# Optimization experiments

Hardware: AMD Instinct MI355X
Metric: run time of the kernel (lower is better)

The kernel has to match this reference:

```python
import jax, jax.numpy as jnp
import numpy as np

NODE_DIM = 128
DEPTH = 4
N_NODES = 10000
N_EDGES = 320000


def setup_inputs() -> dict:
    key = jax.random.key(0)
    ks = jax.random.split(key, 12)
    s = 0.05
    D = NODE_DIM
    inp = {
        'h': jax.random.normal(ks[0], (N_NODES, D), jnp.float32),
        'x': jax.random.normal(ks[1], (N_NODES, 3), jnp.float32),
        'edges': jax.random.randint(ks[2], (2, N_EDGES), 0, N_NODES, jnp.int32),
        # edge_mlp: Linear(2D+1 -> D), SiLU, Linear(D -> D), SiLU  (per layer)
        'edge_w1': jax.random.normal(ks[3], (DEPTH, 2 * D + 1, D), jnp.float32) * s,
        'edge_b1': jnp.zeros((DEPTH, D), jnp.float32),
        'edge_w2': jax.random.normal(ks[4], (DEPTH, D, D), jnp.float32) * s,
        'edge_b2': jnp.zeros((DEPTH, D), jnp.float32),
        # node_mlp: Linear(2D -> D), SiLU, Linear(D -> D)  (per layer)
        'node_w1': jax.random.normal(ks[5], (DEPTH, 2 * D, D), jnp.float32) * s,
        'node_b1': jnp.zeros((DEPTH, D), jnp.float32),
        'node_w2': jax.random.normal(ks[6], (DEPTH, D, D), jnp.float32) * s,
        'node_b2': jnp.zeros((DEPTH, D), jnp.float32),
        # coord_mlp (only used by last layer, update_coords=True):
        # Linear(D -> D), SiLU, Linear(D -> 1, bias=False)
        'coord_w1': jax.random.normal(ks[7], (D, D), jnp.float32) * s,
        'coord_b1': jnp.zeros((D,), jnp.float32),
        'coord_w2': jax.random.normal(ks[8], (D, 1), jnp.float32) * s,
    }
    return inp


def reference(h, x, edges, edge_w1, edge_b1, edge_w2, edge_b2,
              node_w1, node_b1, node_w2, node_b2,
              coord_w1, coord_b1, coord_w2):
    silu = jax.nn.silu
    row, col = edges[0], edges[1]
    n = h.shape[0]
    for i in range(DEPTH):
        # coord2radial
        coord_diff = x[row] - x[col]                       # [E, 3]
        radial = jnp.sum(coord_diff * coord_diff, axis=-1, keepdims=True)  # [E, 1]
        # edge_model: m_ij = edge_mlp([h_i, h_j, radial])
        feat = jnp.concatenate([h[row], h[col], radial], axis=-1)  # [E, 2D+1]
        m = silu(feat @ edge_w1[i] + edge_b1[i])
        m = silu(m @ edge_w2[i] + edge_b2[i])              # [E, D]
        # coord_model (only last layer, coords_agg='mean')
        if i == DEPTH - 1:
            w = silu(m @ coord_w1 + coord_b1) @ coord_w2   # [E, 1]
            trans = coord_diff * w                          # [E, 3]
            agg = jax.ops.segment_sum(trans, row, num_segments=n)
            cnt = jax.ops.segment_sum(jnp.ones((row.shape[0], 1), trans.dtype),
                                      row, num_segments=n)
            x = x + agg / jnp.maximum(cnt, 1.0)
        # node_model: h = h + node_mlp([h, sum_j m_ij])  (residual=True)
        magg = jax.ops.segment_sum(m, row, num_segments=n)  # [N, D]
        hin = jnp.concatenate([h, magg], axis=-1)           # [N, 2D]
        out = silu(hin @ node_w1[i] + node_b1[i]) @ node_w2[i] + node_b2[i]
        h = h + out
    return h, x
```

## Files before the change

### kernel.cpp

```cpp
#include <hip/hip_runtime.h>

#define NND 10000
#define NE  320000
#define DD  128
#define NDEPTH 4
#define TE  64

typedef __attribute__((ext_vector_type(8))) short s8b;
typedef __attribute__((ext_vector_type(4))) float f4;
typedef unsigned short u16;
typedef unsigned int   u32;

__device__ __forceinline__ u16 f2b(float f) {
    u32 u = __builtin_bit_cast(u32, f);
    u32 r = (u + 0x7fffu + ((u >> 16) & 1u)) >> 16;
    return (u16)r;
}

__device__ __forceinline__ float b2f(u16 b) {
    u32 u = (u32)b << 16;
    return __builtin_bit_cast(float, u);
}

__device__ __forceinline__ u32 cvt_pk(float lo, float hi) {
    u32 r;
    asm("v_cvt_pk_bf16_f32 %0, %1, %2" : "=v"(r) : "v"(lo), "v"(hi));
    return r;
}

__device__ __forceinline__ float silu_f(float v) {
    return v / (1.0f + __expf(-v));
}

__device__ __forceinline__ s8b frag_a(const u16* rowp, int g) {
    union { s8b v; uint2 u2[2]; } r;
    r.u2[0] = *(const uint2*)(rowp + 4 * g);
    r.u2[1] = *(const uint2*)(rowp + 16 + 4 * g);
    return r.v;
}

__device__ __forceinline__ f4 mfma16(s8b a, s8b b, f4 c) {
    return __builtin_amdgcn_mfma_f32_16x16x32_bf16(a, b, c, 0, 0, 0);
}

__global__ __launch_bounds__(256) void egnn_pack(
    const float* __restrict__ ew1, const float* __restrict__ ew2,
    const float* __restrict__ nw1, const float* __restrict__ nw2,
    const float* __restrict__ cw1, u16* __restrict__ pw)
{
    int t = blockIdx.x * 256 + threadIdx.x;
    if (t >= 25 * 16384) return;
    int mat = t >> 14;
    int r   = t & 16383;
    int kt  = r >> 12;
    int nt  = (r >> 9) & 7;
    int lane= (r >> 3) & 63;
    int j   = r & 7;
    int g = lane >> 4, l15 = lane & 15;
    int k = kt * 32 + ((j < 4) ? (4 * g + j) : (16 + 4 * g + (j - 4)));
    int n = nt * 16 + l15;
    float v;
    if (mat < 24) {
        int layer = mat / 6, tp = mat % 6;
        switch (tp) {
            case 0: v = ew1[((size_t)layer * 257 + k) * DD + n]; break;
            case 1: v = ew1[((size_t)layer * 257 + 128 + k) * DD + n]; break;
            case 2: v = ew2[((size_t)layer * 128 + k) * DD + n]; break;
            case 3: v = nw1[((size_t)layer * 256 + k) * DD + n]; break;
            case 4: v = nw1[((size_t)layer * 256 + 128 + k) * DD + n]; break;
            default: v = nw2[((size_t)layer * 128 + k) * DD + n]; break;
        }
    } else {
        v = cw1[(size_t)k * DD + n];
    }
    pw[t] = f2b(v);
}

__global__ __launch_bounds__(256) void egnn_init(
    const float* __restrict__ h, u16* __restrict__ hb)
{
    int i = blockIdx.x * 256 + threadIdx.x;
    size_t base = (size_t)i * 4;
    if (base >= (size_t)NND * DD) return;
    float4 v = *(const float4*)(h + base);
    union { u16 s[4]; uint2 u; } t2;
    t2.s[0] = f2b(v.x); t2.s[1] = f2b(v.y); t2.s[2] = f2b(v.z); t2.s[3] = f2b(v.w);
    *(uint2*)(hb + base) = t2.u;
}

__global__ __launch_bounds__(256) void egnn_count(
    const int* __restrict__ edges, int* __restrict__ cnts)
{
    int e = blockIdx.x * 256 + threadIdx.x;
    if (e < NE) atomicAdd(&cnts[edges[e]], 1);
}

__global__ __launch_bounds__(1024) void egnn_scan(
    const int* __restrict__ cnts, int* __restrict__ off, int* __restrict__ cursor)
{
    __shared__ int part[1024];
    const int t = threadIdx.x;
    const int base = t * 10;
    int s = 0;
    #pragma unroll
    for (int j = 0; j < 10; ++j) {
        int i = base + j;
        s += (i < NND) ? cnts[i] : 0;
    }
    part[t] = s;
    __syncthreads();
    for (int d = 1; d < 1024; d <<= 1) {
        int v = (t >= d) ? part[t - d] : 0;
        __syncthreads();
        part[t] += v;
        __syncthreads();
    }
    int run = (t == 0) ? 0 : part[t - 1];
    #pragma unroll
    for (int j = 0; j < 10; ++j) {
        int i = base + j;
        if (i <= NND) { off[i] = run; cursor[i] = run; }
        if (i < NND) run += cnts[i];
    }
}

__global__ __launch_bounds__(256) void egnn_scatter(
    const int* __restrict__ edges, int* __restrict__ cursor,
    int* __restrict__ perm, int* __restrict__ rowsorted)
{
    int e = blockIdx.x * 256 + threadIdx.x;
    if (e >= NE) return;
    int r = edges[e];
    int p = atomicAdd(&cursor[r], 1);
    perm[p] = e;
    rowsorted[p] = r;
}

__global__ __launch_bounds__(256) void egnn_pre0(
    const u16* __restrict__ hb, const u16* __restrict__ pw,
    float* __restrict__ Pb, float* __restrict__ Qb)
{
    __shared__ __attribute__((aligned(16))) u16 tH[64][136];
    const int tid = threadIdx.x;
    const int n0  = blockIdx.x * 64;

    #pragma unroll
    for (int it = 0; it < 4; ++it) {
        int idx = tid + it * 256;
        int el = idx >> 4, part = idx & 15;
        int node = n0 + el;
        if (node < NND) {
            *(uint4*)&tH[el][part * 8] = *(const uint4*)(hb + (size_t)node * DD + part * 8);
        } else {
            uint4 z = {0u, 0u, 0u, 0u};
            *(uint4*)&tH[el][part * 8] = z;
        }
    }
    __syncthreads();

    const int wv = tid >> 6, lane = tid & 63;
    const int g = lane >> 4, l15 = lane & 15;
    const int wrow = wv * 16;

    f4 accP[8], accQ[8];
    #pragma unroll
    for (int nt = 0; nt < 8; ++nt) { accP[nt] = f4{0.f,0.f,0.f,0.f}; accQ[nt] = f4{0.f,0.f,0.f,0.f}; }
    const u16* pwa = pw;
    const u16* pwb = pw + 16384;
    #pragma unroll
    for (int kt = 0; kt < 4; ++kt) {
        s8b a = frag_a(&tH[wrow + l15][kt * 32], g);
        const u16* ba = pwa + (size_t)kt * 4096 + lane * 8;
        const u16* bb = pwb + (size_t)kt * 4096 + lane * 8;
        #pragma unroll
        for (int nt = 0; nt < 8; ++nt) {
            accP[nt] = mfma16(a, *(const s8b*)(ba + nt * 512), accP[nt]);
            accQ[nt] = mfma16(a, *(const s8b*)(bb + nt * 512), accQ[nt]);
        }
    }
    #pragma unroll
    for (int nt = 0; nt < 8; ++nt) {
        int n = nt * 16 + l15;
        #pragma unroll
        for (int r = 0; r < 4; ++r) {
            int node = n0 + wrow + g * 4 + r;
            if (node < NND) {
                Pb[(size_t)node * DD + n] = accP[nt][r];
                Qb[(size_t)node * DD + n] = accQ[nt][r];
            }
        }
    }
}

__global__ __launch_bounds__(256, 6) void egnn_edge(
    const float* __restrict__ Pb, const float* __restrict__ Qb,
    const float* __restrict__ xin,
    const int* __restrict__ edges,
    const int* __restrict__ perm, const int* __restrict__ rowsorted,
    const u16* __restrict__ pw,
    const float* __restrict__ ew1, const float* __restrict__ eb1,
    const float* __restrict__ eb2, const float* __restrict__ cb1,
    const float* __restrict__ cw2,
    float* __restrict__ magg, float* __restrict__ aggx,
    int layer, int last)
{
    __shared__ __attribute__((aligned(16))) u16 tA[TE][136];
    __shared__ float rad[TE];
    __shared__ float cdf[TE][3];
    __shared__ int   ridx[TE];
    __shared__ int   cidx[TE];
    __shared__ unsigned char segflag[TE + 1];

    const int tid = threadIdx.x;
    const int p0  = blockIdx.x * TE;

    if (tid < TE) {
        int p = p0 + tid;
        int e = perm[p];
        int r = rowsorted[p];
        int c = edges[NE + e];
        ridx[tid] = r; cidx[tid] = c;
        float d0 = xin[r * 3 + 0] - xin[c * 3 + 0];
        float d1 = xin[r * 3 + 1] - xin[c * 3 + 1];
        float d2 = xin[r * 3 + 2] - xin[c * 3 + 2];
        rad[tid] = d0 * d0 + d1 * d1 + d2 * d2;
        cdf[tid][0] = d0; cdf[tid][1] = d1; cdf[tid][2] = d2;
    }
    __syncthreads();

    if (tid < TE) {
        segflag[tid] = (tid == 0) || (ridx[tid] != ridx[tid - 1]);
        if (tid == 0) segflag[TE] = 1;
    }

    {
        const int cg = tid & 15;
        const int rg = tid >> 4;
        const float* b1p = eb1 + (size_t)layer * DD + cg * 8;
        const float* wrp = ew1 + ((size_t)layer * 257 + 256) * DD + cg * 8;
        float4 b0 = *(const float4*)(b1p);
        float4 b4 = *(const float4*)(b1p + 4);
        float4 w0 = *(const float4*)(wrp);
        float4 w4 = *(const float4*)(wrp + 4);
        #pragma unroll
        for (int k = 0; k < 4; ++k) {
            int row = rg + 16 * k;
            int rn = ridx[row], cn = cidx[row];
            float rd = rad[row];
            const float* pp = Pb + (size_t)rn * DD + cg * 8;
            const float* qq = Qb + (size_t)cn * DD + cg * 8;
            float4 pa = *(const float4*)(pp);
            float4 pc = *(const float4*)(pp + 4);
            float4 qa = *(const float4*)(qq);
            float4 qc = *(const float4*)(qq + 4);
            float v0 = silu_f(pa.x + qa.x + b0.x + rd * w0.x);
            float v1 = silu_f(pa.y + qa.y + b0.y + rd * w0.y);
            float v2 = silu_f(pa.z + qa.z + b0.z + rd * w0.z);
            float v3 = silu_f(pa.w + qa.w + b0.w + rd * w0.w);
            float v4 = silu_f(pc.x + qc.x + b4.x + rd * w4.x);
            float v5 = silu_f(pc.y + qc.y + b4.y + rd * w4.y);
            float v6 = silu_f(pc.z + qc.z + b4.z + rd * w4.z);
            float v7 = silu_f(pc.w + qc.w + b4.w + rd * w4.w);
            union { u32 w[4]; uint4 u; } cv;
            cv.w[0] = cvt_pk(v0, v1);
            cv.w[1] = cvt_pk(v2, v3);
            cv.w[2] = cvt_pk(v4, v5);
            cv.w[3] = cvt_pk(v6, v7);
            *(uint4*)&tA[row][cg * 8] = cv.u;
        }
    }
    __syncthreads();

    const int wv = tid >> 6, lane = tid & 63;
    const int g = lane >> 4, l15 = lane & 15;
    const int wrow = wv * 16;

    f4 acc2[8];
    #pragma unroll
    for (int nt = 0; nt < 8; ++nt) acc2[nt] = f4{0.f, 0.f, 0.f, 0.f};
    const u16* pw2 = pw + (size_t)(layer * 6 + 2) * 16384;
    #pragma unroll
    for (int kt = 0; kt < 4; ++kt) {
        s8b a = frag_a(&tA[wrow + l15][kt * 32], g);
        const u16* pb = pw2 + (size_t)kt * 4096 + lane * 8;
        #pragma unroll
        for (int nt = 0; nt < 8; ++nt) {
            s8b b = *(const s8b*)(pb + nt * 512);
            acc2[nt] = mfma16(a, b, acc2[nt]);
        }
    }
    {
        const float* b2 = eb2 + (size_t)layer * DD;
        #pragma unroll
        for (int nt = 0; nt < 8; ++nt) {
            int n = nt * 16 + l15;
            float bb = b2[n];
            #pragma unroll
            for (int r = 0; r < 4; ++r) {
                int er = wrow + g * 4 + r;
                float v = silu_f(acc2[nt][r] + bb);
                tA[er][n] = f2b(v);
            }
        }
    }
    __syncthreads();

    {
        int cg2 = tid & 63;
        int r0  = wv * 16;
        float s0 = 0.f, s1 = 0.f;
        #pragma unroll
        for (int i = 0; i < 16; ++i) {
            int row = r0 + i;
            u32 v = *(const u32*)&tA[row][cg2 * 2];
            s0 += b2f((u16)(v & 0xffffu));
            s1 += b2f((u16)(v >> 16));
            if (segflag[row + 1] || i == 15) {
                float* mg = &magg[(size_t)ridx[row] * DD + cg2 * 2];
                atomicAdd(mg, s0);
                atomicAdd(mg + 1, s1);
                s0 = 0.f; s1 = 0.f;
            }
        }
    }

    if (last) {
        f4 acc3[8];
        #pragma unroll
        for (int nt = 0; nt < 8; ++nt) acc3[nt] = f4{0.f, 0.f, 0.f, 0.f};
        const u16* pwc = pw + (size_t)24 * 16384;
        #pragma unroll
        for (int kt = 0; kt < 4; ++kt) {
            s8b a = frag_a(&tA[wrow + l15][kt * 32], g);
            const u16* pb = pwc + (size_t)kt * 4096 + lane * 8;
            #pragma unroll
            for (int nt = 0; nt < 8; ++nt) {
                s8b b = *(const s8b*)(pb + nt * 512);
                acc3[nt] = mfma16(a, b, acc3[nt]);
            }
        }
        float p[4];
        #pragma unroll
        for (int r = 0; r < 4; ++r) p[r] = 0.f;
        #pragma unroll
        for (int nt = 0; nt < 8; ++nt) {
            int n = nt * 16 + l15;
            float bb = cb1[n], w2 = cw2[n];
            #pragma unroll
            for (int r = 0; r < 4; ++r)
                p[r] += silu_f(acc3[nt][r] + bb) * w2;
        }
        #pragma unroll
        for (int off = 1; off < 16; off <<= 1) {
            #pragma unroll
            for (int r = 0; r < 4; ++r)
                p[r] += __shfl_xor(p[r], off);
        }
        if (l15 == 0) {
            #pragma unroll
            for (int r = 0; r < 4; ++r) {
                int er = wrow + 4 * g + r;
                int rn = ridx[er];
                float w = p[r];
                atomicAdd(&aggx[rn * 3 + 0], cdf[er][0] * w);
                atomicAdd(&aggx[rn * 3 + 1], cdf[er][1] * w);
                atomicAdd(&aggx[rn * 3 + 2], cdf[er][2] * w);
            }
        }
    }
}

__global__ __launch_bounds__(256) void egnn_node(
    const u16* __restrict__ hb, const float* __restrict__ resid,
    const float* __restrict__ magg, const u16* __restrict__ pw,
    const float* __restrict__ nb1, const float* __restrict__ nb2,
    float* __restrict__ out_h, u16* __restrict__ hb_out,
    float* __restrict__ Pb, float* __restrict__ Qb,
    int layer, int last)
{
    __shared__ __attribute__((aligned(16))) u16 tH[64][136];
    __shared__ __attribute__((aligned(16))) u16 tM[64][136];
    const int tid = threadIdx.x;
    const int n0  = blockIdx.x * 64;

    #pragma unroll
    for (int it = 0; it < 4; ++it) {
        int idx = tid + it * 256;
        int el = idx >> 4, part = idx & 15;
        int node = n0 + el;
        if (node < NND) {
            *(uint4*)&tH[el][part * 8] = *(const uint4*)(hb + (size_t)node * DD + part * 8);
            const float* ms = magg + (size_t)node * DD + part * 8;
            float4 m0 = *(const float4*)(ms);
            float4 m1 = *(const float4*)(ms + 4);
            union { u32 w[4]; uint4 u; } cv;
            cv.w[0] = cvt_pk(m0.x, m0.y);
            cv.w[1] = cvt_pk(m0.z, m0.w);
            cv.w[2] = cvt_pk(m1.x, m1.y);
            cv.w[3] = cvt_pk(m1.z, m1.w);
            *(uint4*)&tM[el][part * 8] = cv.u;
        } else {
            uint4 z = {0u, 0u, 0u, 0u};
            *(uint4*)&tH[el][part * 8] = z;
            *(uint4*)&tM[el][part * 8] = z;
        }
    }
    __syncthreads();

    const int wv = tid >> 6, lane = tid & 63;
    const int g = lane >> 4, l15 = lane & 15;
    const int wrow = wv * 16;

    f4 acc[8];
    #pragma unroll
    for (int nt = 0; nt < 8; ++nt) acc[nt] = f4{0.f, 0.f, 0.f, 0.f};
    const u16* pn1a = pw + (size_t)(layer * 6 + 3) * 16384;
    const u16* pn1b = pw + (size_t)(layer * 6 + 4) * 16384;
    #pragma unroll
    for (int kt = 0; kt < 8; ++kt) {
        const u16 (*tile)[136] = (kt < 4) ? tH : tM;
        const int k0 = (kt & 3) * 32;
        s8b a = frag_a(&tile[wrow + l15][k0], g);
        const u16* pb = ((kt < 4) ? pn1a : pn1b) + (size_t)(kt & 3) * 4096 + lane * 8;
        #pragma unroll
        for (int nt = 0; nt < 8; ++nt) {
            s8b b = *(const s8b*)(pb + nt * 512);
            acc[nt] = mfma16(a, b, acc[nt]);
        }
    }
    {
        const float* b1 = nb1 + (size_t)layer * DD;
        #pragma unroll
        for (int nt = 0; nt < 8; ++nt) {
            int n = nt * 16 + l15;
            float bb = b1[n];
            #pragma unroll
            for (int r = 0; r < 4; ++r) {
                int er = wrow + g * 4 + r;
                tM[er][n] = f2b(silu_f(acc[nt][r] + bb));
            }
        }
    }
    __syncthreads();

    f4 acc2[8];
    #pragma unroll
    for (int nt = 0; nt < 8; ++nt) acc2[nt] = f4{0.f, 0.f, 0.f, 0.f};
    const u16* pn2 = pw + (size_t)(layer * 6 + 5) * 16384;
    #pragma unroll
    for (int kt = 0; kt < 4; ++kt) {
        s8b a = frag_a(&tM[wrow + l15][kt * 32], g);
        const u16* pb = pn2 + (size_t)kt * 4096 + lane * 8;
        #pragma unroll
        for (int nt = 0; nt < 8; ++nt) {
            s8b b = *(const s8b*)(pb + nt * 512);
            acc2[nt] = mfma16(a, b, acc2[nt]);
        }
    }
    {
        const float* b2 = nb2 + (size_t)layer * DD;
        #pragma unroll
        for (int nt = 0; nt < 8; ++nt) {
            int n = nt * 16 + l15;
            float bb = b2[n];
            #pragma unroll
            for (int r = 0; r < 4; ++r) {
                int er = wrow + g * 4 + r;
                int node = n0 + er;
                if (node < NND) {
                    float v = acc2[nt][r] + bb + resid[(size_t)node * DD + n];
                    out_h[(size_t)node * DD + n] = v;
                    if (!last) {
                        u16 hv = f2b(v);
                        hb_out[(size_t)node * DD + n] = hv;
                        tH[er][n] = hv;
                    }
                } else if (!last) {
                    tH[er][n] = 0;
                }
            }
        }
    }

    if (!last) {
        __syncthreads();
        f4 accP[8], accQ[8];
        #pragma unroll
        for (int nt = 0; nt < 8; ++nt) { accP[nt] = f4{0.f,0.f,0.f,0.f}; accQ[nt] = f4{0.f,0.f,0.f,0.f}; }
        const u16* pwa = pw + (size_t)((layer + 1) * 6 + 0) * 16384;
        const u16* pwb = pw + (size_t)((layer + 1) * 6 + 1) * 16384;
        #pragma unroll
        for (int kt = 0; kt < 4; ++kt) {
            s8b a = frag_a(&tH[wrow + l15][kt * 32], g);
            const u16* ba = pwa + (size_t)kt * 4096 + lane * 8;
            const u16* bb = pwb + (size_t)kt * 4096 + lane * 8;
            #pragma unroll
            for (int nt = 0; nt < 8; ++nt) {
                accP[nt] = mfma16(a, *(const s8b*)(ba + nt * 512), accP[nt]);
                accQ[nt] = mfma16(a, *(const s8b*)(bb + nt * 512), accQ[nt]);
            }
        }
        #pragma unroll
        for (int nt = 0; nt < 8; ++nt) {
            int n = nt * 16 + l15;
            #pragma unroll
            for (int r = 0; r < 4; ++r) {
                int node = n0 + wrow + g * 4 + r;
                if (node < NND) {
                    Pb[(size_t)node * DD + n] = accP[nt][r];
                    Qb[(size_t)node * DD + n] = accQ[nt][r];
                }
            }
        }
    }
}

__global__ __launch_bounds__(256) void egnn_coord_out(
    const float* __restrict__ xin, const float* __restrict__ aggx,
    const int* __restrict__ off, float* __restrict__ out_x)
{
    int i = blockIdx.x * 256 + threadIdx.x;
    if (i >= NND) return;
    float c = (float)(off[i + 1] - off[i]);
    float inv = 1.0f / fmaxf(c, 1.0f);
    out_x[i * 3 + 0] = xin[i * 3 + 0] + aggx[i * 3 + 0] * inv;
    out_x[i * 3 + 1] = xin[i * 3 + 1] + aggx[i * 3 + 1] * inv;
    out_x[i * 3 + 2] = xin[i * 3 + 2] + aggx[i * 3 + 2] * inv;
}

extern "C" void kernel_launch(void* const* d_in, const int* in_sizes, int n_in,
                              void* d_out, int out_size, void* d_ws, size_t ws_size,
                              hipStream_t stream) {
    const float* h   = (const float*)d_in[0];
    const float* x   = (const float*)d_in[1];
    const int*  edges= (const int*)d_in[2];
    const float* ew1 = (const float*)d_in[3];
    const float* eb1 = (const float*)d_in[4];
    const float* ew2 = (const float*)d_in[5];
    const float* eb2 = (const float*)d_in[6];
    const float* nw1 = (const float*)d_in[7];
    const float* nb1 = (const float*)d_in[8];
    const float* nw2 = (const float*)d_in[9];
    const float* nb2 = (const float*)d_in[10];
    const float* cw1 = (const float*)d_in[11];
    const float* cb1 = (const float*)d_in[12];
    const float* cw2 = (const float*)d_in[13];

    char* ws = (char*)d_ws;
    u16*   hb   = (u16*)  (ws);
    float* magg = (float*)(ws + 2560000);
    float* aggx = (float*)(ws + 7680000);
    u16*   pw   = (u16*)  (ws + 7800064);
    int*   cnts = (int*)  (ws + 8619264);
    int*   off  = (int*)  (ws + 8659280);
    int*   curs = (int*)  (ws + 8699296);
    int*   perm = (int*)  (ws + 8739312);
    int*   rows = (int*)  (ws + 10019312);
    float* Pb   = (float*)(ws + 11299312);
    float* Qb   = (float*)(ws + 16419312);

    float* out_h = (float*)d_out;
    float* out_x = out_h + (size_t)NND * DD;

    egnn_pack<<<1600, 256, 0, stream>>>(ew1, ew2, nw1, nw2, cw1, pw);
    egnn_init<<<1250, 256, 0, stream>>>(h, hb);
    hipMemsetAsync(aggx, 0, 120064, stream);
    hipMemsetAsync(cnts, 0, 40016, stream);

    egnn_count<<<1250, 256, 0, stream>>>(edges, cnts);
    egnn_scan<<<1, 1024, 0, stream>>>(cnts, off, curs);
    egnn_scatter<<<1250, 256, 0, stream>>>(edges, curs, perm, rows);
    egnn_pre0<<<(NND + 63) / 64, 256, 0, stream>>>(hb, pw, Pb, Qb);

    for (int i = 0; i < NDEPTH; ++i) {
        int last = (i == NDEPTH - 1);
        hipMemsetAsync(magg, 0, (size_t)NND * DD * 4, stream);
        egnn_edge<<<NE / TE, 256, 0, stream>>>(Pb, Qb, x, edges, perm, rows, pw,
                                               ew1, eb1, eb2, cb1, cw2,
                                               magg, aggx, i, last);
        const float* resid = (i == 0) ? h : (const float*)out_h;
        egnn_node<<<(NND + 63) / 64, 256, 0, stream>>>(hb, resid, magg, pw, nb1, nb2,
                                                       out_h, hb, Pb, Qb, i, last);
    }
    egnn_coord_out<<<40, 256, 0, stream>>>(x, aggx, off, out_x);
}
```

Measured before the change: 573.4 us.

## Replace atomic message aggregation with per-edge buffer and segmented reduction kernel

```diff
diff --git a/kernel.cpp b/kernel.cpp
--- a/kernel.cpp
+++ b/kernel.cpp
@@ -20,6 +20,11 @@
 __device__ __forceinline__ float b2f(u16 b) {
     u32 u = (u32)b << 16;
     return __builtin_bit_cast(float, u);
+}
+
+__device__ __forceinline__ void bpair(u32 v, float& lo, float& hi) {
+    lo = __builtin_bit_cast(float, v << 16);
+    hi = __builtin_bit_cast(float, v & 0xffff0000u);
 }
 
 __device__ __forceinline__ u32 cvt_pk(float lo, float hi) {
@@ -126,14 +131,14 @@
 
 __global__ __launch_bounds__(256) void egnn_scatter(
     const int* __restrict__ edges, int* __restrict__ cursor,
-    int* __restrict__ perm, int* __restrict__ rowsorted)
+    int* __restrict__ rows, int* __restrict__ cols)
 {
     int e = blockIdx.x * 256 + threadIdx.x;
     if (e >= NE) return;
     int r = edges[e];
     int p = atomicAdd(&cursor[r], 1);
-    perm[p] = e;
-    rowsorted[p] = r;
+    rows[p] = r;
+    cols[p] = edges[NE + e];
 }
 
 __global__ __launch_bounds__(256) void egnn_pre0(
@@ -195,14 +200,14 @@
 __global__ __launch_bounds__(256, 6) void egnn_edge(
     const float* __restrict__ Pb, const float* __restrict__ Qb,
     const float* __restrict__ xin,
-    const int* __restrict__ edges,
-    const int* __restrict__ perm, const int* __restrict__ rowsorted,
+    const int* __restrict__ rows, const int* __restrict__ cols,
     const u16* __restrict__ pw,
     const float* __restrict__ ew1, const float* __restrict__ eb1,
     const float* __restrict__ eb2, const float* __restrict__ cb1,
     const float* __restrict__ cw2,
-    float* __restrict__ magg, float* __restrict__ aggx,
-    int layer, int last)
+    float* __restrict__ maggf, u16* __restrict__ m2seg,
+    float* __restrict__ aggx,
+    int layer, int last, int segmode)
 {
     __shared__ __attribute__((aligned(16))) u16 tA[TE][136];
     __shared__ float rad[TE];
@@ -216,9 +221,8 @@
 
     if (tid < TE) {
         int p = p0 + tid;
-        int e = perm[p];
-        int r = rowsorted[p];
-        int c = edges[NE + e];
+        int r = rows[p];
+        int c = cols[p];
         ridx[tid] = r; cidx[tid] = c;
         float d0 = xin[r * 3 + 0] - xin[c * 3 + 0];
         float d1 = xin[r * 3 + 1] - xin[c * 3 + 1];
@@ -228,7 +232,7 @@
     }
     __syncthreads();
 
-    if (tid < TE) {
+    if (!segmode && tid < TE) {
         segflag[tid] = (tid == 0) || (ridx[tid] != ridx[tid - 1]);
         if (tid == 0) segflag[TE] = 1;
     }
@@ -305,7 +309,15 @@
     }
     __syncthreads();
 
-    {
+    if (segmode) {
+        #pragma unroll
+        for (int it = 0; it < 4; ++it) {
+            int idx = tid + it * 256;
+            int el = idx >> 4, part = idx & 15;
+            *(uint4*)(m2seg + (size_t)(p0 + el) * DD + part * 8) =
+                *(const uint4*)&tA[el][part * 8];
+        }
+    } else {
         int cg2 = tid & 63;
         int r0  = wv * 16;
         float s0 = 0.f, s1 = 0.f;
@@ -316,7 +328,7 @@
             s0 += b2f((u16)(v & 0xffffu));
             s1 += b2f((u16)(v >> 16));
             if (segflag[row + 1] || i == 15) {
-                float* mg = &magg[(size_t)ridx[row] * DD + cg2 * 2];
+                float* mg = &maggf[(size_t)ridx[row] * DD + cg2 * 2];
                 atomicAdd(mg, s0);
                 atomicAdd(mg + 1, s1);
                 s0 = 0.f; s1 = 0.f;
@@ -370,13 +382,40 @@
     }
 }
 
+__global__ __launch_bounds__(256) void egnn_agg(
+    const u16* __restrict__ m2seg, const int* __restrict__ off,
+    u16* __restrict__ maggb)
+{
+    int t = blockIdx.x * 256 + threadIdx.x;
+    if (t >= NND * 16) return;
+    int node = t >> 4, part = t & 15;
+    int a = off[node], b = off[node + 1];
+    float s0 = 0.f, s1 = 0.f, s2 = 0.f, s3 = 0.f, s4 = 0.f, s5 = 0.f, s6 = 0.f, s7 = 0.f;
+    const u16* base = m2seg + (size_t)part * 8;
+    for (int p = a; p < b; ++p) {
+        uint4 v = *(const uint4*)(base + (size_t)p * DD);
+        float lo, hi;
+        bpair(v.x, lo, hi); s0 += lo; s1 += hi;
+        bpair(v.y, lo, hi); s2 += lo; s3 += hi;
+        bpair(v.z, lo, hi); s4 += lo; s5 += hi;
+        bpair(v.w, lo, hi); s6 += lo; s7 += hi;
+    }
+    union { u32 w[4]; uint4 u; } cv;
+    cv.w[0] = cvt_pk(s0, s1);
+    cv.w[1] = cvt_pk(s2, s3);
+    cv.w[2] = cvt_pk(s4, s5);
+    cv.w[3] = cvt_pk(s6, s7);
+    *(uint4*)(maggb + (size_t)node * DD + part * 8) = cv.u;
+}
+
 __global__ __launch_bounds__(256) void egnn_node(
     const u16* __restrict__ hb, const float* __restrict__ resid,
-    const float* __restrict__ magg, const u16* __restrict__ pw,
+    const u16* __restrict__ maggb, const float* __restrict__ maggf,
+    const u16* __restrict__ pw,
     const float* __restrict__ nb1, const float* __restrict__ nb2,
     float* __restrict__ out_h, u16* __restrict__ hb_out,
     float* __restrict__ Pb, float* __restrict__ Qb,
-    int layer, int last)
+    int layer, int last, int segmode)
 {
     __shared__ __attribute__((aligned(16))) u16 tH[64][136];
     __shared__ __attribute__((aligned(16))) u16 tM[64][136];
@@ -390,15 +429,19 @@
         int node = n0 + el;
         if (node < NND) {
             *(uint4*)&tH[el][part * 8] = *(const uint4*)(hb + (size_t)node * DD + part * 8);
-            const float* ms = magg + (size_t)node * DD + part * 8;
-            float4 m0 = *(const float4*)(ms);
-            float4 m1 = *(const float4*)(ms + 4);
-            union { u32 w[4]; uint4 u; } cv;
-            cv.w[0] = cvt_pk(m0.x, m0.y);
-            cv.w[1] = cvt_pk(m0.z, m0.w);
-            cv.w[2] = cvt_pk(m1.x, m1.y);
-            cv.w[3] = cvt_pk(m1.z, m1.w);
-            *(uint4*)&tM[el][part * 8] = cv.u;
+            if (segmode) {
+                *(uint4*)&tM[el][part * 8] = *(const uint4*)(maggb + (size_t)node * DD + part * 8);
+            } else {
+                const float* ms = maggf + (size_t)node * DD + part * 8;
+                float4 m0 = *(const float4*)(ms);
+                float4 m1 = *(const float4*)(ms + 4);
+                union { u32 w[4]; uint4 u; } cv;
+                cv.w[0] = cvt_pk(m0.x, m0.y);
+                cv.w[1] = cvt_pk(m0.z, m0.w);
+                cv.w[2] = cvt_pk(m1.x, m1.y);
+                cv.w[3] = cvt_pk(m1.z, m1.w);
+                *(uint4*)&tM[el][part * 8] = cv.u;
+            }
         } else {
             uint4 z = {0u, 0u, 0u, 0u};
             *(uint4*)&tH[el][part * 8] = z;
@@ -547,17 +590,21 @@
     const float* cw2 = (const float*)d_in[13];
 
     char* ws = (char*)d_ws;
-    u16*   hb   = (u16*)  (ws);
-    float* magg = (float*)(ws + 2560000);
-    float* aggx = (float*)(ws + 7680000);
-    u16*   pw   = (u16*)  (ws + 7800064);
-    int*   cnts = (int*)  (ws + 8619264);
-    int*   off  = (int*)  (ws + 8659280);
-    int*   curs = (int*)  (ws + 8699296);
-    int*   perm = (int*)  (ws + 8739312);
-    int*   rows = (int*)  (ws + 10019312);
-    float* Pb   = (float*)(ws + 11299312);
-    float* Qb   = (float*)(ws + 16419312);
+    u16*   hb    = (u16*)  (ws);
+    u16*   pw    = (u16*)  (ws + 2560000);
+    int*   cnts  = (int*)  (ws + 3379200);
+    int*   off   = (int*)  (ws + 3419216);
+    int*   curs  = (int*)  (ws + 3459232);
+    int*   rows  = (int*)  (ws + 3499248);
+    int*   cols  = (int*)  (ws + 4779248);
+    float* aggx  = (float*)(ws + 6059248);
+    float* Pb    = (float*)(ws + 6179312);
+    float* Qb    = (float*)(ws + 11299312);
+    u16*   maggb = (u16*)  (ws + 16419312);
+    float* maggf = (float*)(ws + 18979312);
+    u16*   m2seg = (u16*)  (ws + 24099312);
+
+    const int segmode = (ws_size >= 106019312ull) ? 1 : 0;
 
     float* out_h = (float*)d_out;
     float* out_x = out_h + (size_t)NND * DD;
@@ -569,18 +616,21 @@
 
     egnn_count<<<1250, 256, 0, stream>>>(edges, cnts);
     egnn_scan<<<1, 1024, 0, stream>>>(cnts, off, curs);
-    egnn_scatter<<<1250, 256, 0, stream>>>(edges, curs, perm, rows);
+    egnn_scatter<<<1250, 256, 0, stream>>>(edges, curs, rows, cols);
     egnn_pre0<<<(NND + 63) / 64, 256, 0, stream>>>(hb, pw, Pb, Qb);
 
     for (int i = 0; i < NDEPTH; ++i) {
         int last = (i == NDEPTH - 1);
-        hipMemsetAsync(magg, 0, (size_t)NND * DD * 4, stream);
-        egnn_edge<<<NE / TE, 256, 0, stream>>>(Pb, Qb, x, edges, perm, rows, pw,
+        if (!segmode) hipMemsetAsync(maggf, 0, (size_t)NND * DD * 4, stream);
+        egnn_edge<<<NE / TE, 256, 0, stream>>>(Pb, Qb, x, rows, cols, pw,
                                                ew1, eb1, eb2, cb1, cw2,
-                                               magg, aggx, i, last);
+                                               maggf, m2seg, aggx, i, last, segmode);
+        if (segmode)
+            egnn_agg<<<(NND * 16) / 256, 256, 0, stream>>>(m2seg, off, maggb);
         const float* resid = (i == 0) ? h : (const float*)out_h;
-        egnn_node<<<(NND + 63) / 64, 256, 0, stream>>>(hb, resid, magg, pw, nb1, nb2,
-                                                       out_h, hb, Pb, Qb, i, last);
+        egnn_node<<<(NND + 63) / 64, 256, 0, stream>>>(hb, resid, maggb, maggf,
+                                                       pw, nb1, nb2,
+                                                       out_h, hb, Pb, Qb, i, last, segmode);
     }
     egnn_coord_out<<<40, 256, 0, stream>>>(x, aggx, off, out_x);
 }
```

Result: slower. 625.3 us (+9.1%).

## Double edge tile to 128 with 512 threads, store sorted cols, simplify segment reduction

Applied to the files above, without the earlier changes.

```diff
diff --git a/kernel.cpp b/kernel.cpp
--- a/kernel.cpp
+++ b/kernel.cpp
@@ -4,7 +4,7 @@
 #define NE  320000
 #define DD  128
 #define NDEPTH 4
-#define TE  64
+#define TE  128
 
 typedef __attribute__((ext_vector_type(8))) short s8b;
 typedef __attribute__((ext_vector_type(4))) float f4;
@@ -126,14 +126,14 @@
 
 __global__ __launch_bounds__(256) void egnn_scatter(
     const int* __restrict__ edges, int* __restrict__ cursor,
-    int* __restrict__ perm, int* __restrict__ rowsorted)
+    int* __restrict__ rows, int* __restrict__ cols)
 {
     int e = blockIdx.x * 256 + threadIdx.x;
     if (e >= NE) return;
     int r = edges[e];
     int p = atomicAdd(&cursor[r], 1);
-    perm[p] = e;
-    rowsorted[p] = r;
+    rows[p] = r;
+    cols[p] = edges[NE + e];
 }
 
 __global__ __launch_bounds__(256) void egnn_pre0(
@@ -192,11 +192,10 @@
     }
 }
 
-__global__ __launch_bounds__(256, 6) void egnn_edge(
+__global__ __launch_bounds__(512, 4) void egnn_edge(
     const float* __restrict__ Pb, const float* __restrict__ Qb,
     const float* __restrict__ xin,
-    const int* __restrict__ edges,
-    const int* __restrict__ perm, const int* __restrict__ rowsorted,
+    const int* __restrict__ rows, const int* __restrict__ cols,
     const u16* __restrict__ pw,
     const float* __restrict__ ew1, const float* __restrict__ eb1,
     const float* __restrict__ eb2, const float* __restrict__ cb1,
@@ -216,9 +215,8 @@
 
     if (tid < TE) {
         int p = p0 + tid;
-        int e = perm[p];
-        int r = rowsorted[p];
-        int c = edges[NE + e];
+        int r = rows[p];
+        int c = cols[p];
         ridx[tid] = r; cidx[tid] = c;
         float d0 = xin[r * 3 + 0] - xin[c * 3 + 0];
         float d1 = xin[r * 3 + 1] - xin[c * 3 + 1];
@@ -244,7 +242,7 @@
         float4 w4 = *(const float4*)(wrp + 4);
         #pragma unroll
         for (int k = 0; k < 4; ++k) {
-            int row = rg + 16 * k;
+            int row = rg + 32 * k;
             int rn = ridx[row], cn = cidx[row];
             float rd = rad[row];
             const float* pp = Pb + (size_t)rn * DD + cg * 8;
@@ -305,21 +303,16 @@
     }
     __syncthreads();
 
-    {
-        int cg2 = tid & 63;
-        int r0  = wv * 16;
-        float s0 = 0.f, s1 = 0.f;
-        #pragma unroll
-        for (int i = 0; i < 16; ++i) {
-            int row = r0 + i;
-            u32 v = *(const u32*)&tA[row][cg2 * 2];
-            s0 += b2f((u16)(v & 0xffffu));
-            s1 += b2f((u16)(v >> 16));
-            if (segflag[row + 1] || i == 15) {
-                float* mg = &magg[(size_t)ridx[row] * DD + cg2 * 2];
-                atomicAdd(mg, s0);
-                atomicAdd(mg + 1, s1);
-                s0 = 0.f; s1 = 0.f;
+    if (tid < 256) {
+        int col  = tid & 127;
+        int half = tid >> 7;
+        int r0 = half * 64, r1 = r0 + 64;
+        float s = 0.f;
+        for (int row = r0; row < r1; ++row) {
+            s += b2f(tA[row][col]);
+            if (segflag[row + 1] || row == r1 - 1) {
+                atomicAdd(&magg[(size_t)ridx[row] * DD + col], s);
+                s = 0.f;
             }
         }
     }
@@ -548,16 +541,16 @@
 
     char* ws = (char*)d_ws;
     u16*   hb   = (u16*)  (ws);
-    float* magg = (float*)(ws + 2560000);
-    float* aggx = (float*)(ws + 7680000);
-    u16*   pw   = (u16*)  (ws + 7800064);
-    int*   cnts = (int*)  (ws + 8619264);
-    int*   off  = (int*)  (ws + 8659280);
-    int*   curs = (int*)  (ws + 8699296);
-    int*   perm = (int*)  (ws + 8739312);
-    int*   rows = (int*)  (ws + 10019312);
-    float* Pb   = (float*)(ws + 11299312);
-    float* Qb   = (float*)(ws + 16419312);
+    u16*   pw   = (u16*)  (ws + 2560000);
+    int*   cnts = (int*)  (ws + 3379200);
+    int*   off  = (int*)  (ws + 3419216);
+    int*   curs = (int*)  (ws + 3459232);
+    int*   rows = (int*)  (ws + 3499248);
+    int*   cols = (int*)  (ws + 4779248);
+    float* aggx = (float*)(ws + 6059248);
+    float* Pb   = (float*)(ws + 6179312);
+    float* Qb   = (float*)(ws + 11299312);
+    float* magg = (float*)(ws + 16419312);
 
     float* out_h = (float*)d_out;
     float* out_x = out_h + (size_t)NND * DD;
@@ -569,13 +562,13 @@
 
     egnn_count<<<1250, 256, 0, stream>>>(edges, cnts);
     egnn_scan<<<1, 1024, 0, stream>>>(cnts, off, curs);
-    egnn_scatter<<<1250, 256, 0, stream>>>(edges, curs, perm, rows);
+    egnn_scatter<<<1250, 256, 0, stream>>>(edges, curs, rows, cols);
     egnn_pre0<<<(NND + 63) / 64, 256, 0, stream>>>(hb, pw, Pb, Qb);
 
     for (int i = 0; i < NDEPTH; ++i) {
         int last = (i == NDEPTH - 1);
         hipMemsetAsync(magg, 0, (size_t)NND * DD * 4, stream);
-        egnn_edge<<<NE / TE, 256, 0, stream>>>(Pb, Qb, x, edges, perm, rows, pw,
+        egnn_edge<<<NE / TE, 512, 0, stream>>>(Pb, Qb, x, rows, cols, pw,
                                                ew1, eb1, eb2, cb1, cw2,
                                                magg, aggx, i, last);
         const float* resid = (i == 0) ? h : (const float*)out_h;
```

Measured after the change: 587.9 us. 2.5% more time.
